# Kernel optimization log

Measured on AMD Instinct MI355X. Metric: run time of the kernel, lower is better.

## Reference

```python
import jax, jax.numpy as jnp
import numpy as np

_EPS = 1e-5
_K = 3  # spatial kernel size (partitions of adjacency)


def _build_A():
    num_node = 24
    self_link = [(i, i) for i in range(num_node)]
    neighbor = [(1, 0), (2, 0), (3, 0), (4, 1), (5, 2), (6, 3), (7, 4), (8, 5), (9, 6),
                (10, 7), (11, 8), (12, 9), (13, 9), (14, 9), (15, 12), (16, 13), (17, 14),
                (18, 16), (19, 17), (20, 18), (21, 19), (22, 20), (23, 21)]
    edges = self_link + neighbor
    Ab = np.zeros((num_node, num_node))
    for i, j in edges:
        Ab[j, i] = 1
        Ab[i, j] = 1
    max_hop = 1
    hop_dis = np.full((num_node, num_node), np.inf)
    transfer = [np.linalg.matrix_power(Ab, d) for d in range(max_hop + 1)]
    arrive = np.stack(transfer) > 0
    for d in range(max_hop, -1, -1):
        hop_dis[arrive[d]] = d
    adjacency = np.zeros((num_node, num_node))
    for hop in range(max_hop + 1):
        adjacency[hop_dis == hop] = 1
    Dl = adjacency.sum(0)
    Dn = np.zeros_like(adjacency)
    for i in range(num_node):
        if Dl[i] > 0:
            Dn[i, i] = Dl[i] ** (-1)
    AD = adjacency @ Dn
    center = 0
    As = []
    for hop in range(max_hop + 1):
        a_root = np.zeros_like(AD)
        a_close = np.zeros_like(AD)
        a_further = np.zeros_like(AD)
        for i in range(num_node):
            for j in range(num_node):
                if hop_dis[j, i] == hop:
                    if hop_dis[j, center] == hop_dis[i, center]:
                        a_root[j, i] = AD[j, i]
                    elif hop_dis[j, center] > hop_dis[i, center]:
                        a_close[j, i] = AD[j, i]
                    else:
                        a_further[j, i] = AD[j, i]
        if hop == 0:
            As.append(a_root)
        else:
            As.append(a_root + a_close)
            As.append(a_further)
    return np.stack(As).astype(np.float32)  # [3, 24, 24]


def setup_inputs() -> dict:
    key = jax.random.key(0)
    cnt = [0]
    def nk():
        cnt[0] += 1
        return jax.random.fold_in(key, cnt[0])
    def rn(shape, scale=1.0):
        return scale * jax.random.normal(nk(), shape, jnp.float32)
    B, T, N, C = 32, 256, 24, 3
    inp = {}
    inp['x'] = rn((B, T, N, C))
    inp['A'] = jnp.asarray(_build_A())
    inp['data_bn_g'] = 1.0 + 0.1 * rn((N * C,))
    inp['data_bn_b'] = 0.1 * rn((N * C,))
    for li in range(3):
        inp['ei%d' % li] = 1.0 + 0.05 * rn((_K, 24, 24))  # edge importance
    chans = [(C, 256), (256, 128), (128, 64)]
    for li, (ci, co) in enumerate(chans):
        p = 'l%d_' % li
        inp[p + 'gcn_w'] = rn((co * _K, ci), 1.0 / np.sqrt(ci))
        inp[p + 'gcn_b'] = 0.01 * rn((co * _K,))
        inp[p + 'bn1_g'] = 1.0 + 0.1 * rn((co,))
        inp[p + 'bn1_b'] = 0.1 * rn((co,))
        inp[p + 'tcn_w'] = rn((co, co, 5, 1), 1.0 / np.sqrt(co * 5))
        inp[p + 'tcn_b'] = 0.01 * rn((co,))
        inp[p + 'bn2_g'] = 1.0 + 0.1 * rn((co,))
        inp[p + 'bn2_b'] = 0.1 * rn((co,))
        if li > 0:  # residual 1x1 conv + BN when in_channels != out_channels
            inp[p + 'res_w'] = rn((co, ci), 1.0 / np.sqrt(ci))
            inp[p + 'res_b'] = 0.01 * rn((co,))
            inp[p + 'res_bn_g'] = 1.0 + 0.1 * rn((co,))
            inp[p + 'res_bn_b'] = 0.1 * rn((co,))
    inp['fcn_w'] = rn((6, 64), 1.0 / np.sqrt(64))
    inp['fcn_b'] = 0.01 * rn((6,))
    return inp


def _bn(x, g, b):
    # eval-mode BatchNorm2d, running_mean=0, running_var=1; x: [B,C,T,V]
    inv = 1.0 / np.sqrt(1.0 + _EPS)
    return x * (inv * g)[None, :, None, None] + b[None, :, None, None]


def _gcn(x, w, b, Aeff):
    # x: [B,Cin,T,V]; w: [K*Cout,Cin]; Aeff: [K,V,V]
    y = jnp.einsum('bctv,oc->botv', x, w) + b[None, :, None, None]
    Bn, KC, Tn, V = y.shape
    y = y.reshape(Bn, _K, KC // _K, Tn, V)
    return jnp.einsum('bkctv,kvw->bctw', y, Aeff)


def _tconv(x, w, b):
    # temporal conv kernel (5,1), pad (2,0); NCHW
    y = jax.lax.conv_general_dilated(x, w, window_strides=(1, 1),
                                     padding=((2, 2), (0, 0)),
                                     dimension_numbers=('NCHW', 'OIHW', 'NCHW'))
    return y + b[None, :, None, None]


def _layer(x, Aeff, gw, gb, g1, b1, tw, tb, g2, b2, res):
    y = _gcn(x, gw, gb, Aeff)
    y = jax.nn.relu(_bn(y, g1, b1))
    y = _bn(_tconv(y, tw, tb), g2, b2) + res  # dropout is identity in eval
    return jax.nn.relu(y)


def reference(x, A, data_bn_g, data_bn_b, ei0, ei1, ei2,
              l0_gcn_w, l0_gcn_b, l0_bn1_g, l0_bn1_b, l0_tcn_w, l0_tcn_b, l0_bn2_g, l0_bn2_b,
              l1_gcn_w, l1_gcn_b, l1_bn1_g, l1_bn1_b, l1_tcn_w, l1_tcn_b, l1_bn2_g, l1_bn2_b,
              l1_res_w, l1_res_b, l1_res_bn_g, l1_res_bn_b,
              l2_gcn_w, l2_gcn_b, l2_bn1_g, l2_bn1_b, l2_tcn_w, l2_tcn_b, l2_bn2_g, l2_bn2_b,
              l2_res_w, l2_res_b, l2_res_bn_g, l2_res_bn_b,
              fcn_w, fcn_b):
    B, T, N, C = x.shape
    # data_bn over N*C channels (eval mode)
    xb = x.transpose(0, 2, 3, 1).reshape(B, N * C, T)
    inv = 1.0 / np.sqrt(1.0 + _EPS)
    xb = xb * (inv * data_bn_g)[None, :, None] + data_bn_b[None, :, None]
    h = xb.reshape(B, N, C, T).transpose(0, 2, 3, 1)  # [B,C,T,V]
    # layer 0: no residual
    h = _layer(h, A * ei0, l0_gcn_w, l0_gcn_b, l0_bn1_g, l0_bn1_b,
               l0_tcn_w, l0_tcn_b, l0_bn2_g, l0_bn2_b, 0.0)
    # layer 1: 1x1 conv + BN residual (256 -> 128)
    r1 = _bn(jnp.einsum('bctv,oc->botv', h, l1_res_w) + l1_res_b[None, :, None, None],
             l1_res_bn_g, l1_res_bn_b)
    h = _layer(h, A * ei1, l1_gcn_w, l1_gcn_b, l1_bn1_g, l1_bn1_b,
               l1_tcn_w, l1_tcn_b, l1_bn2_g, l1_bn2_b, r1)
    # layer 2: 1x1 conv + BN residual (128 -> 64)
    r2 = _bn(jnp.einsum('bctv,oc->botv', h, l2_res_w) + l2_res_b[None, :, None, None],
             l2_res_bn_g, l2_res_bn_b)
    h = _layer(h, A * ei2, l2_gcn_w, l2_gcn_b, l2_bn1_g, l2_bn1_b,
               l2_tcn_w, l2_tcn_b, l2_bn2_g, l2_bn2_b, r2)
    out = jnp.einsum('bctv,oc->botv', h, fcn_w) + fcn_b[None, :, None, None]
    return out.transpose(0, 2, 3, 1)  # [B,T,V,6]
```

## Files before the change

kernel.cpp:

```cpp
#include <hip/hip_runtime.h>

typedef _Float16 half8 __attribute__((ext_vector_type(8)));
typedef _Float16 half2v __attribute__((ext_vector_type(2)));
typedef float floatx16 __attribute__((ext_vector_type(16)));

static constexpr int gT = 256;
static constexpr int gV = 24;
static constexpr int gN = gT * gV;
static constexpr float BN_INV = 0.99999500003749969f;

#define GLOAD_LDS16(g, l)                                            \
  __builtin_amdgcn_global_load_lds(                                  \
      (const __attribute__((address_space(1))) unsigned int*)(g),    \
      (__attribute__((address_space(3))) unsigned int*)(l), 16, 0, 0)

__global__ __launch_bounds__(256) void k_prep_aeff(
    const float* __restrict__ A, const float* __restrict__ e0,
    const float* __restrict__ e1, const float* __restrict__ e2,
    float* __restrict__ aeff, float* __restrict__ csum)
{
  int tid = blockIdx.x * 256 + threadIdx.x;
  if (tid < 3 * 1728) {
    int l = tid / 1728, r = tid % 1728;
    const float* e = (l == 0) ? e0 : ((l == 1) ? e1 : e2);
    aeff[tid] = A[r] * e[r];
  }
  if (tid < 3 * 72) {
    int l = tid / 72, r = tid % 72;
    int k = r / 24, w = r % 24;
    const float* e = (l == 0) ? e0 : ((l == 1) ? e1 : e2);
    float s = 0.f;
    for (int v = 0; v < 24; ++v) { int idx = (k * 24 + v) * 24 + w; s += A[idx] * e[idx]; }
    csum[tid] = s;
  }
}

__global__ __launch_bounds__(256) void k_prep_twf(
    const float* __restrict__ tw, _Float16* __restrict__ out, int CI, int KT)
{
  int g = blockIdx.x * 256 + threadIdx.x;
  int fid = g >> 6, lane = g & 63;
  int pl = fid & 1;
  int f2 = fid >> 1;
  int dt = f2 % 5;
  int f3 = f2 / 5;
  int ks = f3 & 1;
  int f4 = f3 >> 1;
  int kt = f4 % KT;
  int mt = f4 / KT;
  int m = mt * 32 + (lane & 31);
  int kb = kt * 32 + ks * 16 + ((lane >> 5) << 3);
  half8 o;
#pragma unroll
  for (int e = 0; e < 8; ++e) {
    float v = tw[((size_t)m * CI + (kb + e)) * 5 + dt];
    _Float16 h = (_Float16)v;
    o[e] = pl ? (_Float16)(v - (float)h) : h;
  }
  *(half8*)(out + ((size_t)fid * 64 + lane) * 8) = o;
}

__global__ __launch_bounds__(256) void k_pack_wz(
    const float* __restrict__ Wg, const float* __restrict__ Wr,
    _Float16* __restrict__ out, int CIN, int KT, int M3)
{
  int g = blockIdx.x * 256 + threadIdx.x;
  int fid = g >> 6, lane = g & 63;
  int pl = fid & 1;
  int ks = (fid >> 1) & 1;
  int rest = fid >> 2;
  int kt = rest % KT;
  int mt = rest / KT;
  int m = mt * 32 + (lane & 31);
  int kb = kt * 32 + ks * 16 + ((lane >> 5) << 3);
  const float* row = (m < M3) ? (Wg + (size_t)m * CIN) : (Wr + (size_t)(m - M3) * CIN);
  half8 o;
#pragma unroll
  for (int e = 0; e < 8; ++e) {
    float v = row[kb + e];
    _Float16 h = (_Float16)v;
    o[e] = pl ? (_Float16)(v - (float)h) : h;
  }
  *(half8*)(out + ((size_t)fid * 64 + lane) * 8) = o;
}

__global__ __launch_bounds__(256) void k_gcn0(
    const float* __restrict__ x,
    const float* __restrict__ aeff,
    const float* __restrict__ csum,
    const float* __restrict__ dbg, const float* __restrict__ dbb,
    const float* __restrict__ W0,
    const float* __restrict__ gb0,
    const float* __restrict__ g1, const float* __restrict__ b1,
    _Float16* __restrict__ yh, _Float16* __restrict__ yl,
    int b0)
{
  __shared__ float xbn[72];
  __shared__ float XA[216];
  __shared__ float WL[2304];
  __shared__ float tile[256 * 25];
  int t0 = blockIdx.x * 4, bl = blockIdx.y, tid = threadIdx.x;
  int b = b0 + bl;
  int c = tid;

  for (int i = tid; i < 2304; i += 256) WL[i] = W0[i];

  for (int tr = 0; tr < 4; ++tr) {
    int t = t0 + tr;
    __syncthreads();
    if (tid < 72) {
      int v = tid / 3, cin = tid % 3;
      float xv = x[(((size_t)b * gT + t) * gV + v) * 3 + cin];
      xbn[cin * 24 + v] = xv * (BN_INV * dbg[tid]) + dbb[tid];
    }
    __syncthreads();
    if (tid < 216) {
      int k = tid / 72, r = tid % 72, ci = r / 24, w = r % 24;
      const float* Ak = aeff + k * 576;
      float s = 0.f;
#pragma unroll
      for (int v = 0; v < 24; ++v) s += xbn[ci * 24 + v] * Ak[v * 24 + w];
      XA[tid] = s;
    }
    __syncthreads();

    float acc[24];
#pragma unroll
    for (int w = 0; w < 24; ++w) acc[w] = 0.f;
#pragma unroll
    for (int k = 0; k < 3; ++k) {
#pragma unroll
      for (int ci = 0; ci < 3; ++ci) {
        float wv = WL[(k * 256 + c) * 3 + ci];
#pragma unroll
        for (int w = 0; w < 24; ++w) acc[w] += wv * XA[(k * 3 + ci) * 24 + w];
      }
      float gv = gb0[k * 256 + c];
#pragma unroll
      for (int w = 0; w < 24; ++w) acc[w] += gv * csum[k * 24 + w];
    }
    float s1 = BN_INV * g1[c], o1 = b1[c];
#pragma unroll
    for (int w = 0; w < 24; ++w) tile[c * 25 + w] = fmaxf(acc[w] * s1 + o1, 0.f);
    __syncthreads();

    size_t nb = ((size_t)bl * gN + (size_t)t * 24);
    _Float16* dhB = yh + nb * 256;
    _Float16* dlB = yl + nb * 256;
#pragma unroll
    for (int it = 0; it < 3; ++it) {
      int idx = it * 256 + tid;
      int w = idx >> 5;
      int c0 = (idx & 31) * 8;
      half8 vh, vl;
#pragma unroll
      for (int q = 0; q < 8; ++q) {
        float v = tile[(c0 + q) * 25 + w];
        _Float16 hh = (_Float16)v;
        vh[q] = hh;
        vl[q] = (_Float16)(v - (float)hh);
      }
      *(half8*)(dhB + (size_t)w * 256 + c0) = vh;
      *(half8*)(dlB + (size_t)w * 256 + c0) = vl;
    }
  }
}

template <int CIN, int COUT>
__global__ __launch_bounds__(512) void k_gcnfuse(
    const _Float16* __restrict__ pH, const _Float16* __restrict__ pL,
    const _Float16* __restrict__ Wf,
    const float* __restrict__ aeffL, const float* __restrict__ csumL,
    const float* __restrict__ gb, const float* __restrict__ g1, const float* __restrict__ b1,
    _Float16* __restrict__ oH, _Float16* __restrict__ oL,
    float* __restrict__ res_out,
    int NBc)
{
  constexpr int KT = CIN / 32;
  constexpr int M = 4 * COUT;
  constexpr int M3 = 3 * COUT;
  constexpr int MT = M / 256;
  constexpr int BSTG_FL = 2 * 2 * 96 * 40 / 2;
  constexpr int ZLW = M * 25;
  constexpr int UNIW = (ZLW > BSTG_FL) ? ZLW : BSTG_FL;
  __shared__ float UNI[UNIW];
  __shared__ float AL[1728];
  __shared__ float csL[72];
  __shared__ __align__(16) _Float16 YST[24 * COUT * 2];
  _Float16* Bb = (_Float16*)UNI;
  float* ZL = UNI;

  int tid = threadIdx.x, w = tid >> 6, lane = tid & 63;
  int n0 = blockIdx.x * 96;

  for (int i = tid; i < 1728; i += 512) AL[i] = aeffL[i];
  if (tid < 72) csL[tid] = csumL[tid];

  floatx16 acc[MT][3] = {};

  uint4 pf[2];
  auto PREF = [&](int kt) {
#pragma unroll
    for (int it = 0; it < 2; ++it) {
      int task = it * 512 + tid;
      if (task < 768) {
        int row = task >> 3, pl = (task >> 2) & 1, seg = task & 3;
        pf[it] = *(const uint4*)((pl ? pL : pH) + (size_t)(n0 + row) * CIN + kt * 32 + seg * 8);
      }
    }
  };
  auto WRITE = [&](int buf) {
#pragma unroll
    for (int it = 0; it < 2; ++it) {
      int task = it * 512 + tid;
      if (task < 768) {
        int row = task >> 3, pl = (task >> 2) & 1, seg = task & 3;
        *(uint4*)(Bb + (((size_t)buf * 2 + pl) * 96 + row) * 40 + seg * 8) = pf[it];
      }
    }
  };

  PREF(0); WRITE(0); __syncthreads();
  int cur = 0;
  for (int kt = 0; kt < KT; ++kt) {
    if (kt + 1 < KT) PREF(kt + 1);
    const _Float16* BH = Bb + (size_t)(cur * 2 + 0) * 96 * 40;
    const _Float16* BL2 = Bb + (size_t)(cur * 2 + 1) * 96 * 40;
    __builtin_amdgcn_s_setprio(1);
#pragma unroll
    for (int ks = 0; ks < 2; ++ks) {
      int koff = ks * 16 + ((lane >> 5) << 3);
      int rowb = lane & 31;
      half8 bh[3], bl[3];
#pragma unroll
      for (int nf = 0; nf < 3; ++nf) {
        bh[nf] = *(const half8*)(BH + (rowb + nf * 32) * 40 + koff);
        bl[nf] = *(const half8*)(BL2 + (rowb + nf * 32) * 40 + koff);
      }
#pragma unroll
      for (int mti = 0; mti < MT; ++mti) {
        int mt = w * MT + mti;
        int fid = ((mt * KT + kt) * 2 + ks) * 2;
        half8 ah = *(const half8*)(Wf + ((size_t)fid * 64 + lane) * 8);
        half8 al = *(const half8*)(Wf + ((size_t)(fid + 1) * 64 + lane) * 8);
#pragma unroll
        for (int nf = 0; nf < 3; ++nf) {
          acc[mti][nf] = __builtin_amdgcn_mfma_f32_32x32x16_f16(ah, bh[nf], acc[mti][nf], 0, 0, 0);
          acc[mti][nf] = __builtin_amdgcn_mfma_f32_32x32x16_f16(ah, bl[nf], acc[mti][nf], 0, 0, 0);
          acc[mti][nf] = __builtin_amdgcn_mfma_f32_32x32x16_f16(al, bh[nf], acc[mti][nf], 0, 0, 0);
        }
      }
    }
    __builtin_amdgcn_s_setprio(0);
    if (kt + 1 < KT) WRITE(cur ^ 1);
    __syncthreads();
    cur ^= 1;
  }

  constexpr int SUBS = 512 / COUT;
  constexpr int WR = 24 / SUBS;
  int c = tid & (COUT - 1);
  int w0 = (tid / COUT) * WR;
  float s1 = BN_INV * g1[c], o1 = b1[c];
  float gv0 = gb[c], gv1 = gb[COUT + c], gv2 = gb[2 * COUT + c];

  for (int tr = 0; tr < 4; ++tr) {
    __syncthreads();
#pragma unroll
    for (int mti = 0; mti < MT; ++mti) {
#pragma unroll
      for (int nf = 0; nf < 3; ++nf) {
        int nloc = nf * 32 + (lane & 31) - tr * 24;
        if (nloc >= 0 && nloc < 24) {
          int mb_ = (w * MT + mti) * 32 + 4 * (lane >> 5);
#pragma unroll
          for (int r = 0; r < 16; ++r)
            ZL[(mb_ + (r & 3) + 8 * (r >> 2)) * 25 + nloc] = acc[mti][nf][r];
        }
      }
    }
    __syncthreads();
    float y[WR];
#pragma unroll
    for (int j = 0; j < WR; ++j) y[j] = 0.f;
#pragma unroll
    for (int k = 0; k < 3; ++k) {
#pragma unroll
      for (int v = 0; v < 24; ++v) {
        float zr = ZL[(k * COUT + c) * 25 + v];
        const float* ap = &AL[k * 576 + v * 24 + w0];
#pragma unroll
        for (int j = 0; j < WR; ++j) y[j] += zr * ap[j];
      }
    }
#pragma unroll
    for (int j = 0; j < WR; ++j) {
      int ww = w0 + j;
      float bias = gv0 * csL[ww] + gv1 * csL[24 + ww] + gv2 * csL[48 + ww];
      float yv = fmaxf((y[j] + bias) * s1 + o1, 0.f);
      _Float16 h = (_Float16)yv;
      YST[ww * COUT + c] = h;
      YST[24 * COUT + ww * COUT + c] = (_Float16)(yv - (float)h);
    }
    __syncthreads();
    constexpr int QT = 24 * COUT / 8;
    size_t nbase = (size_t)n0 + tr * 24;
    for (int idx = tid; idx < 2 * QT; idx += 512) {
      int plane = idx / QT, q = idx - plane * QT;
      _Float16* dst = (plane ? oL : oH) + nbase * COUT + q * 8;
      *(half8*)dst = *(half8*)(YST + plane * 24 * COUT + q * 8);
    }
    for (int idx = tid; idx < COUT * 6; idx += 512) {
      int cc = idx / 6, q = idx - cc * 6;
      float4 v4;
      v4.x = ZL[(M3 + cc) * 25 + 4 * q + 0];
      v4.y = ZL[(M3 + cc) * 25 + 4 * q + 1];
      v4.z = ZL[(M3 + cc) * 25 + 4 * q + 2];
      v4.w = ZL[(M3 + cc) * 25 + 4 * q + 3];
      *(float4*)(res_out + (size_t)cc * NBc + nbase + 4 * q) = v4;
    }
  }
}

template <int CIO, int MF, bool FUSE_FC>
__global__ __launch_bounds__(512) void k_tcn_mfma(
    const _Float16* __restrict__ yH, const _Float16* __restrict__ yL,
    const _Float16* __restrict__ Apack,
    const float* __restrict__ tb, const float* __restrict__ g2, const float* __restrict__ b2,
    const float* __restrict__ Zres,
    const float* __restrict__ rb, const float* __restrict__ rg, const float* __restrict__ rbb,
    _Float16* __restrict__ oH, _Float16* __restrict__ oL,
    const float* __restrict__ fw, const float* __restrict__ fb,
    float* __restrict__ outp, int b0,
    int NBc)
{
  constexpr int KT = CIO / 32;
  constexpr int M = CIO;
  constexpr int NWAVE_M = M / (MF * 32);
  constexpr int NWAVE_N = 8 / NWAVE_M;
  constexpr int NF = 128 / (32 * NWAVE_N);
  constexpr int NROW = 224;
  __shared__ _Float16 Bt[2][NROW * 64];
  __shared__ float scL[CIO], ofL[CIO], tbL[CIO], rscL[CIO], rofL[CIO], rbvL[CIO];
  __shared__ float fwL[FUSE_FC ? 384 : 4];
  int bx = blockIdx.x, bl = blockIdx.z;
  int tid = threadIdx.x, w = tid >> 6, lane = tid & 63;
  int wn = w % NWAVE_N, wm = w / NWAVE_N;
  int n0 = bx * 128;
  bool interior = (bx > 0) && (bx < 47);

  for (int i = tid; i < CIO; i += 512) {
    scL[i] = BN_INV * g2[i]; ofL[i] = b2[i]; tbL[i] = tb[i];
    if (Zres) { rscL[i] = BN_INV * rg[i]; rofL[i] = rbb[i]; rbvL[i] = rb[i]; }
  }
  if (FUSE_FC) { for (int i = tid; i < 384; i += 512) fwL[i] = fw[i]; }

  floatx16 acc[MF][NF] = {};
  const _Float16* ybH = yH + (size_t)bl * gN * CIO;
  const _Float16* ybL = yL + (size_t)bl * gN * CIO;
  int mt_base = wm * MF;

  auto ISSUE = [&](int kt, int buf) {
#pragma unroll
    for (int it = 0; it < 4; ++it) {
      int slot = w * 4 + it;
      if (slot < 28) {
        int T = slot * 64 + lane;
        int r = T >> 3, s = T & 7;
        int sl = s ^ (r & 7);
        int pl = sl >> 2, seg = sl & 3;
        int n = n0 - 48 + r;
        const _Float16* src = (pl ? ybL : ybH) + (size_t)n * CIO + kt * 32 + seg * 8;
        GLOAD_LDS16(src, &Bt[buf][(size_t)slot * 512]);
      }
    }
  };
  auto ISSUE_EDGE = [&](int kt, int buf) {
#pragma unroll
    for (int it = 0; it < 4; ++it) {
      int slot = w * 4 + it;
      if (slot < 28) {
        int T = slot * 64 + lane;
        int r = T >> 3, s = T & 7;
        int sl = s ^ (r & 7);
        int pl = sl >> 2, seg = sl & 3;
        int n = n0 - 48 + r;
        uint4 vv = make_uint4(0u, 0u, 0u, 0u);
        if (n >= 0 && n < gN)
          vv = *(const uint4*)((pl ? ybL : ybH) + (size_t)n * CIO + kt * 32 + seg * 8);
        *(uint4*)(&Bt[buf][(size_t)T * 8]) = vv;
      }
    }
  };
  auto COMPUTE = [&](int kt, int buf) {
    const _Float16* B = &Bt[buf][0];
    __builtin_amdgcn_s_setprio(1);
#pragma unroll
    for (int dt = 0; dt < 5; ++dt) {
#pragma unroll
      for (int ks = 0; ks < 2; ++ks) {
        int seg = ks * 2 + (lane >> 5);
        half8 bh[NF], blv[NF];
#pragma unroll
        for (int nf = 0; nf < NF; ++nf) {
          int rr = wn * (NF * 32) + nf * 32 + dt * 24 + (lane & 31);
          bh[nf]  = *(const half8*)(B + rr * 64 + (((0 + seg) ^ (rr & 7)) * 8));
          blv[nf] = *(const half8*)(B + rr * 64 + (((4 + seg) ^ (rr & 7)) * 8));
        }
#pragma unroll
        for (int mf = 0; mf < MF; ++mf) {
          int fid = ((((mt_base + mf) * KT + kt) * 2 + ks) * 5 + dt) * 2;
          half8 ah = *(const half8*)(Apack + ((size_t)fid * 64 + lane) * 8);
          half8 al = *(const half8*)(Apack + ((size_t)(fid + 1) * 64 + lane) * 8);
#pragma unroll
          for (int nf = 0; nf < NF; ++nf) {
            acc[mf][nf] = __builtin_amdgcn_mfma_f32_32x32x16_f16(ah, bh[nf], acc[mf][nf], 0, 0, 0);
            acc[mf][nf] = __builtin_amdgcn_mfma_f32_32x32x16_f16(ah, blv[nf], acc[mf][nf], 0, 0, 0);
            acc[mf][nf] = __builtin_amdgcn_mfma_f32_32x32x16_f16(al, bh[nf], acc[mf][nf], 0, 0, 0);
          }
        }
      }
    }
    __builtin_amdgcn_s_setprio(0);
  };

  if (interior) {
    ISSUE(0, 0);
    int cur = 0;
    for (int kt = 0; kt < KT; ++kt) {
      __builtin_amdgcn_sched_barrier(0);
      if (kt + 1 < KT) ISSUE(kt + 1, cur ^ 1);
      __builtin_amdgcn_sched_barrier(0);
      if (kt + 1 < KT) asm volatile("s_waitcnt vmcnt(4)" ::: "memory");
      else             asm volatile("s_waitcnt vmcnt(0)" ::: "memory");
      __builtin_amdgcn_sched_barrier(0);
      __builtin_amdgcn_s_barrier();
      __builtin_amdgcn_sched_barrier(0);
      COMPUTE(kt, cur);
      asm volatile("s_waitcnt lgkmcnt(0)" ::: "memory");
      __builtin_amdgcn_sched_barrier(0);
      __builtin_amdgcn_s_barrier();
      cur ^= 1;
    }
  } else {
    for (int kt = 0; kt < KT; ++kt) {
      __syncthreads();
      ISSUE_EDGE(kt, 0);
      __syncthreads();
      COMPUTE(kt, 0);
    }
  }

  int blgN = bl * gN;
#pragma unroll
  for (int mf = 0; mf < MF; ++mf) {
    int m32 = wm * MF * 32 + mf * 32 + 4 * (lane >> 5);
#pragma unroll
    for (int nf = 0; nf < NF; ++nf) {
      int n = n0 + wn * (NF * 32) + nf * 32 + (lane & 31);
      size_t nflat = (size_t)blgN + n;
#pragma unroll
      for (int r = 0; r < 16; ++r) {
        int co = m32 + (r & 3) + 8 * (r >> 2);
        float z = (acc[mf][nf][r] + tbL[co]) * scL[co] + ofL[co];
        if (Zres) z += (Zres[(size_t)co * NBc + nflat] + rbvL[co]) * rscL[co] + rofL[co];
        acc[mf][nf][r] = fmaxf(z, 0.f);
      }
    }
  }

  if constexpr (FUSE_FC) {
    __syncthreads();
    float* FC = (float*)&Bt[0][0];
    float p[6];
#pragma unroll
    for (int o = 0; o < 6; ++o) p[o] = 0.f;
    int m32 = wm * 32 + 4 * (lane >> 5);
#pragma unroll
    for (int r = 0; r < 16; ++r) {
      int co = m32 + (r & 3) + 8 * (r >> 2);
      float z = acc[0][0][r];
#pragma unroll
      for (int o = 0; o < 6; ++o) p[o] += fwL[o * 64 + co] * z;
    }
#pragma unroll
    for (int o = 0; o < 6; ++o) p[o] += __shfl_xor(p[o], 32);
    if (lane < 32) {
      int nloc = wn * 32 + lane;
#pragma unroll
      for (int o = 0; o < 6; ++o)
        FC[(wm * 128 + nloc) * 6 + o] = p[o];
    }
    __syncthreads();
    for (int idx = tid; idx < 768; idx += 512) {
      int nloc = idx / 6, o = idx % 6;
      float val = fb[o] + FC[nloc * 6 + o] + FC[(128 + nloc) * 6 + o];
      int n = n0 + nloc;
      int t = n / 24, v = n % 24;
      outp[(((size_t)(b0 + bl) * gT + t) * gV + v) * 6 + o] = val;
    }
  } else {
    constexpr int CPB = CIO / 2;
    constexpr int NHALF = (128 * (CPB + 1) * 4 > 2 * NROW * 64 * 2) ? 2 : 1;
    constexpr int ROWS_P = 128 / NHALF;
    constexpr int PITCH = CPB + 1;
    uint* ST = (uint*)&Bt[0][0];
    uint* oH32 = (uint*)oH;
    uint* oL32 = (uint*)oL;
    constexpr int QITERS = ROWS_P * CPB / 4 / 512;

#pragma unroll
    for (int half = 0; half < NHALF; ++half) {
#pragma unroll
      for (int pass = 0; pass < 2; ++pass) {
        __syncthreads();
        if (NHALF == 1 || wn == half) {
          int cl = wm * MF * 32;
#pragma unroll
          for (int mf = 0; mf < MF; ++mf) {
#pragma unroll
            for (int nf = 0; nf < NF; ++nf) {
              int nl = wn * (NF * 32) + nf * 32 + (lane & 31) - half * ROWS_P;
#pragma unroll
              for (int r = 0; r < 16; r += 2) {
                float z0 = acc[mf][nf][r], z1 = acc[mf][nf][r + 1];
                _Float16 a0 = (_Float16)z0, a1 = (_Float16)z1;
                if (pass == 1) { a0 = (_Float16)(z0 - (float)a0); a1 = (_Float16)(z1 - (float)a1); }
                half2v p2; p2[0] = a0; p2[1] = a1;
                int col2 = (cl + mf * 32 + 4 * (lane >> 5) + (r & 3) + 8 * (r >> 2)) >> 1;
                ST[nl * PITCH + col2] = *(uint*)&p2;
              }
            }
          }
        }
        __syncthreads();
        uint* dst = (pass == 0) ? oH32 : oL32;
#pragma unroll
        for (int i = 0; i < QITERS; ++i) {
          int idx = i * 512 + tid;
          int row = idx / (CPB / 4), c4 = (idx % (CPB / 4)) * 4;
          uint4 v;
          v.x = ST[row * PITCH + c4 + 0];
          v.y = ST[row * PITCH + c4 + 1];
          v.z = ST[row * PITCH + c4 + 2];
          v.w = ST[row * PITCH + c4 + 3];
          *(uint4*)(dst + ((size_t)blgN + n0 + half * ROWS_P + row) * (CIO / 2) + c4) = v;
        }
      }
    }
  }
}

extern "C" void kernel_launch(void* const* d_in, const int* in_sizes, int n_in,
                              void* d_out, int out_size, void* d_ws, size_t ws_size,
                              hipStream_t stream) {
  const float* x    = (const float*)d_in[0];
  const float* A    = (const float*)d_in[1];
  const float* dbg  = (const float*)d_in[2];
  const float* dbb  = (const float*)d_in[3];
  const float* ei0  = (const float*)d_in[4];
  const float* ei1  = (const float*)d_in[5];
  const float* ei2  = (const float*)d_in[6];
  const float* w0g  = (const float*)d_in[7];
  const float* gb0  = (const float*)d_in[8];
  const float* g10  = (const float*)d_in[9];
  const float* b10  = (const float*)d_in[10];
  const float* tw0  = (const float*)d_in[11];
  const float* tb0  = (const float*)d_in[12];
  const float* g20  = (const float*)d_in[13];
  const float* b20  = (const float*)d_in[14];
  const float* w1g  = (const float*)d_in[15];
  const float* gb1  = (const float*)d_in[16];
  const float* g11  = (const float*)d_in[17];
  const float* b11  = (const float*)d_in[18];
  const float* tw1  = (const float*)d_in[19];
  const float* tb1  = (const float*)d_in[20];
  const float* g21  = (const float*)d_in[21];
  const float* b21  = (const float*)d_in[22];
  const float* rw1  = (const float*)d_in[23];
  const float* rb1  = (const float*)d_in[24];
  const float* rg1  = (const float*)d_in[25];
  const float* rbb1 = (const float*)d_in[26];
  const float* w2g  = (const float*)d_in[27];
  const float* gb2  = (const float*)d_in[28];
  const float* g12  = (const float*)d_in[29];
  const float* b12  = (const float*)d_in[30];
  const float* tw2  = (const float*)d_in[31];
  const float* tb2  = (const float*)d_in[32];
  const float* g22  = (const float*)d_in[33];
  const float* b22  = (const float*)d_in[34];
  const float* rw2  = (const float*)d_in[35];
  const float* rb2  = (const float*)d_in[36];
  const float* rg2  = (const float*)d_in[37];
  const float* rbb2 = (const float*)d_in[38];
  const float* fw   = (const float*)d_in[39];
  const float* fb   = (const float*)d_in[40];
  float* outp = (float*)d_out;
  float* ws = (float*)d_ws;

  size_t off = 0;
  auto alloc = [&](size_t n) { size_t o = off; off += n; return o; };
  size_t oAE  = alloc(3 * 1728);
  size_t oCS  = alloc(3 * 72);
  size_t oA0  = alloc((size_t)1280 * 512 / 2);
  size_t oA1  = alloc((size_t)320 * 512 / 2);
  size_t oA2  = alloc((size_t)80 * 512 / 2);
  size_t oWz1 = alloc((size_t)512 * 512 / 2);
  size_t oWz2 = alloc((size_t)128 * 512 / 2);
  off = (off + 3) & ~(size_t)3;

  const size_t perBatchBytes = (size_t)gN * 640 * 4;
  int Bc = 32;
  while (Bc > 1 && off * 4 + (size_t)Bc * perBatchBytes > ws_size) Bc >>= 1;
  int NBc = Bc * gN;

  float* B1 = ws + off;
  float* B2 = B1 + (size_t)NBc * 256;
  float* Rb = B2 + (size_t)NBc * 256;
  _Float16* b1h = (_Float16*)B1;
  _Float16* b2h = (_Float16*)B2;
  _Float16* A0 = (_Float16*)(ws + oA0);
  _Float16* A1 = (_Float16*)(ws + oA1);
  _Float16* A2 = (_Float16*)(ws + oA2);
  _Float16* Wz1 = (_Float16*)(ws + oWz1);
  _Float16* Wz2 = (_Float16*)(ws + oWz2);

  k_prep_aeff<<<21, 256, 0, stream>>>(A, ei0, ei1, ei2, ws + oAE, ws + oCS);
  k_prep_twf<<<320, 256, 0, stream>>>(tw0, A0, 256, 8);
  k_prep_twf<<<80, 256, 0, stream>>>(tw1, A1, 128, 4);
  k_prep_twf<<<20, 256, 0, stream>>>(tw2, A2, 64, 2);
  k_pack_wz<<<128, 256, 0, stream>>>(w1g, rw1, Wz1, 256, 8, 384);
  k_pack_wz<<<32, 256, 0, stream>>>(w2g, rw2, Wz2, 128, 4, 192);

  for (int b0 = 0; b0 < 32; b0 += Bc) {
    k_gcn0<<<dim3(gT / 4, Bc), 256, 0, stream>>>(x, ws + oAE, ws + oCS, dbg, dbb,
                                                 w0g, gb0, g10, b10,
                                                 b1h, b1h + (size_t)NBc * 256, b0);
    k_tcn_mfma<256, 2, false><<<dim3(48, 1, Bc), 512, 0, stream>>>(
        b1h, b1h + (size_t)NBc * 256, A0, tb0, g20, b20,
        nullptr, nullptr, nullptr, nullptr,
        b2h, b2h + (size_t)NBc * 256, nullptr, nullptr, nullptr, 0, NBc);
    k_gcnfuse<256, 128><<<dim3(NBc / 96), 512, 0, stream>>>(
        b2h, b2h + (size_t)NBc * 256, Wz1,
        ws + oAE + 1728, ws + oCS + 72, gb1, g11, b11,
        b1h, b1h + (size_t)NBc * 128, Rb, NBc);
    k_tcn_mfma<128, 2, false><<<dim3(48, 1, Bc), 512, 0, stream>>>(
        b1h, b1h + (size_t)NBc * 128, A1, tb1, g21, b21,
        Rb, rb1, rg1, rbb1,
        b2h, b2h + (size_t)NBc * 128, nullptr, nullptr, nullptr, 0, NBc);
    k_gcnfuse<128, 64><<<dim3(NBc / 96), 512, 0, stream>>>(
        b2h, b2h + (size_t)NBc * 128, Wz2,
        ws + oAE + 2 * 1728, ws + oCS + 144, gb2, g12, b12,
        b1h, b1h + (size_t)NBc * 64, Rb, NBc);
    k_tcn_mfma<64, 1, true><<<dim3(48, 1, Bc), 512, 0, stream>>>(
        b1h, b1h + (size_t)NBc * 64, A2, tb2, g22, b22,
        Rb, rb2, rg2, rbb2,
        nullptr, nullptr, fw, fb, outp, b0, NBc);
  }
  (void)in_sizes; (void)n_in; (void)out_size;
}
```

Baseline: 1.323 ms.

## Double TCN tile width to 256 and drop LDS double buffering

The temporal-conv MFMA kernel now computes 256 output positions per block instead of 128. This cuts the 48-row temporal halo overhead per block and halves the grid. The double-buffered async load pipeline is replaced with a single LDS buffer and plain syncthreads between load and compute, which frees LDS for the larger tile but removes the overlap of global loads with MFMA work. The epilogue and the fused FC path are adjusted to the wider tile, and the grid shrinks to 24 blocks per batch, which may reduce occupancy and load balance.

New measurement: 1.645 ms. 24.3% more time.

```diff
diff --git a/kernel.cpp b/kernel.cpp
--- a/kernel.cpp
+++ b/kernel.cpp
@@ -336,18 +336,20 @@
 {
   constexpr int KT = CIO / 32;
   constexpr int M = CIO;
+  constexpr int N_BLK = 256;
   constexpr int NWAVE_M = M / (MF * 32);
   constexpr int NWAVE_N = 8 / NWAVE_M;
-  constexpr int NF = 128 / (32 * NWAVE_N);
-  constexpr int NROW = 224;
-  __shared__ _Float16 Bt[2][NROW * 64];
+  constexpr int NF = N_BLK / (32 * NWAVE_N);
+  constexpr int NROW = 352;
+  constexpr int NSLOT = NROW * 8;
+  __shared__ _Float16 Bt[NROW * 64];
   __shared__ float scL[CIO], ofL[CIO], tbL[CIO], rscL[CIO], rofL[CIO], rbvL[CIO];
   __shared__ float fwL[FUSE_FC ? 384 : 4];
   int bx = blockIdx.x, bl = blockIdx.z;
   int tid = threadIdx.x, w = tid >> 6, lane = tid & 63;
   int wn = w % NWAVE_N, wm = w / NWAVE_N;
-  int n0 = bx * 128;
-  bool interior = (bx > 0) && (bx < 47);
+  int n0 = bx * N_BLK;
+  bool interior = (bx > 0) && (bx < (gN / N_BLK - 1));
 
   for (int i = tid; i < CIO; i += 512) {
     scL[i] = BN_INV * g2[i]; ofL[i] = b2[i]; tbL[i] = tb[i];
@@ -360,27 +362,26 @@
   const _Float16* ybL = yL + (size_t)bl * gN * CIO;
   int mt_base = wm * MF;
 
-  auto ISSUE = [&](int kt, int buf) {
-#pragma unroll
-    for (int it = 0; it < 4; ++it) {
-      int slot = w * 4 + it;
-      if (slot < 28) {
-        int T = slot * 64 + lane;
+  auto ISSUE = [&](int kt) {
+#pragma unroll
+    for (int it = 0; it < 6; ++it) {
+      int base = it * 512 + w * 64;
+      if (base < NSLOT) {
+        int T = base + lane;
         int r = T >> 3, s = T & 7;
         int sl = s ^ (r & 7);
         int pl = sl >> 2, seg = sl & 3;
         int n = n0 - 48 + r;
         const _Float16* src = (pl ? ybL : ybH) + (size_t)n * CIO + kt * 32 + seg * 8;
-        GLOAD_LDS16(src, &Bt[buf][(size_t)slot * 512]);
+        GLOAD_LDS16(src, Bt + (size_t)base * 8);
       }
     }
   };
-  auto ISSUE_EDGE = [&](int kt, int buf) {
-#pragma unroll
-    for (int it = 0; it < 4; ++it) {
-      int slot = w * 4 + it;
-      if (slot < 28) {
-        int T = slot * 64 + lane;
+  auto ISSUE_EDGE = [&](int kt) {
+#pragma unroll
+    for (int it = 0; it < 6; ++it) {
+      int T = it * 512 + tid;
+      if (T < NSLOT) {
         int r = T >> 3, s = T & 7;
         int sl = s ^ (r & 7);
         int pl = sl >> 2, seg = sl & 3;
@@ -388,12 +389,12 @@
         uint4 vv = make_uint4(0u, 0u, 0u, 0u);
         if (n >= 0 && n < gN)
           vv = *(const uint4*)((pl ? ybL : ybH) + (size_t)n * CIO + kt * 32 + seg * 8);
-        *(uint4*)(&Bt[buf][(size_t)T * 8]) = vv;
+        *(uint4*)(Bt + (size_t)T * 8) = vv;
       }
     }
   };
-  auto COMPUTE = [&](int kt, int buf) {
-    const _Float16* B = &Bt[buf][0];
+  auto COMPUTE = [&](int kt) {
+    const _Float16* B = &Bt[0];
     __builtin_amdgcn_s_setprio(1);
 #pragma unroll
     for (int dt = 0; dt < 5; ++dt) {
@@ -424,31 +425,11 @@
     __builtin_amdgcn_s_setprio(0);
   };
 
-  if (interior) {
-    ISSUE(0, 0);
-    int cur = 0;
-    for (int kt = 0; kt < KT; ++kt) {
-      __builtin_amdgcn_sched_barrier(0);
-      if (kt + 1 < KT) ISSUE(kt + 1, cur ^ 1);
-      __builtin_amdgcn_sched_barrier(0);
-      if (kt + 1 < KT) asm volatile("s_waitcnt vmcnt(4)" ::: "memory");
-      else             asm volatile("s_waitcnt vmcnt(0)" ::: "memory");
-      __builtin_amdgcn_sched_barrier(0);
-      __builtin_amdgcn_s_barrier();
-      __builtin_amdgcn_sched_barrier(0);
-      COMPUTE(kt, cur);
-      asm volatile("s_waitcnt lgkmcnt(0)" ::: "memory");
-      __builtin_amdgcn_sched_barrier(0);
-      __builtin_amdgcn_s_barrier();
-      cur ^= 1;
-    }
-  } else {
-    for (int kt = 0; kt < KT; ++kt) {
-      __syncthreads();
-      ISSUE_EDGE(kt, 0);
-      __syncthreads();
-      COMPUTE(kt, 0);
-    }
+  for (int kt = 0; kt < KT; ++kt) {
+    __syncthreads();
+    if (interior) ISSUE(kt); else ISSUE_EDGE(kt);
+    __syncthreads();
+    COMPUTE(kt);
   }
 
   int blgN = bl * gN;
@@ -471,56 +452,60 @@
 
   if constexpr (FUSE_FC) {
     __syncthreads();
-    float* FC = (float*)&Bt[0][0];
-    float p[6];
-#pragma unroll
-    for (int o = 0; o < 6; ++o) p[o] = 0.f;
+    float* FC = (float*)&Bt[0];
     int m32 = wm * 32 + 4 * (lane >> 5);
 #pragma unroll
-    for (int r = 0; r < 16; ++r) {
-      int co = m32 + (r & 3) + 8 * (r >> 2);
-      float z = acc[0][0][r];
-#pragma unroll
-      for (int o = 0; o < 6; ++o) p[o] += fwL[o * 64 + co] * z;
-    }
-#pragma unroll
-    for (int o = 0; o < 6; ++o) p[o] += __shfl_xor(p[o], 32);
-    if (lane < 32) {
-      int nloc = wn * 32 + lane;
-#pragma unroll
-      for (int o = 0; o < 6; ++o)
-        FC[(wm * 128 + nloc) * 6 + o] = p[o];
-    }
-    __syncthreads();
-    for (int idx = tid; idx < 768; idx += 512) {
+    for (int nf = 0; nf < 2; ++nf) {
+      float p[6];
+#pragma unroll
+      for (int o = 0; o < 6; ++o) p[o] = 0.f;
+#pragma unroll
+      for (int r = 0; r < 16; ++r) {
+        int co = m32 + (r & 3) + 8 * (r >> 2);
+        float z = acc[0][nf][r];
+#pragma unroll
+        for (int o = 0; o < 6; ++o) p[o] += fwL[o * 64 + co] * z;
+      }
+#pragma unroll
+      for (int o = 0; o < 6; ++o) p[o] += __shfl_xor(p[o], 32);
+      if (lane < 32) {
+        int nloc = wn * 64 + nf * 32 + lane;
+#pragma unroll
+        for (int o = 0; o < 6; ++o)
+          FC[(wm * 256 + nloc) * 6 + o] = p[o];
+      }
+    }
+    __syncthreads();
+    for (int idx = tid; idx < 1536; idx += 512) {
       int nloc = idx / 6, o = idx % 6;
-      float val = fb[o] + FC[nloc * 6 + o] + FC[(128 + nloc) * 6 + o];
+      float val = fb[o] + FC[nloc * 6 + o] + FC[(256 + nloc) * 6 + o];
       int n = n0 + nloc;
       int t = n / 24, v = n % 24;
       outp[(((size_t)(b0 + bl) * gT + t) * gV + v) * 6 + o] = val;
     }
   } else {
     constexpr int CPB = CIO / 2;
-    constexpr int NHALF = (128 * (CPB + 1) * 4 > 2 * NROW * 64 * 2) ? 2 : 1;
-    constexpr int ROWS_P = 128 / NHALF;
+    constexpr int ROWS_P = (CIO == 256) ? 64 : 128;
+    constexpr int NSEG = N_BLK / ROWS_P;
     constexpr int PITCH = CPB + 1;
-    uint* ST = (uint*)&Bt[0][0];
+    uint* ST = (uint*)&Bt[0];
     uint* oH32 = (uint*)oH;
     uint* oL32 = (uint*)oL;
     constexpr int QITERS = ROWS_P * CPB / 4 / 512;
 
 #pragma unroll
-    for (int half = 0; half < NHALF; ++half) {
+    for (int seg = 0; seg < NSEG; ++seg) {
 #pragma unroll
       for (int pass = 0; pass < 2; ++pass) {
         __syncthreads();
-        if (NHALF == 1 || wn == half) {
-          int cl = wm * MF * 32;
-#pragma unroll
-          for (int mf = 0; mf < MF; ++mf) {
-#pragma unroll
-            for (int nf = 0; nf < NF; ++nf) {
-              int nl = wn * (NF * 32) + nf * 32 + (lane & 31) - half * ROWS_P;
+        int cl = wm * MF * 32;
+#pragma unroll
+        for (int mf = 0; mf < MF; ++mf) {
+#pragma unroll
+          for (int nf = 0; nf < NF; ++nf) {
+            int rbase = wn * (NF * 32) + nf * 32;
+            if (rbase >= seg * ROWS_P && rbase < (seg + 1) * ROWS_P) {
+              int nl = rbase + (lane & 31) - seg * ROWS_P;
 #pragma unroll
               for (int r = 0; r < 16; r += 2) {
                 float z0 = acc[mf][nf][r], z1 = acc[mf][nf][r + 1];
@@ -544,7 +529,7 @@
           v.y = ST[row * PITCH + c4 + 1];
           v.z = ST[row * PITCH + c4 + 2];
           v.w = ST[row * PITCH + c4 + 3];
-          *(uint4*)(dst + ((size_t)blgN + n0 + half * ROWS_P + row) * (CIO / 2) + c4) = v;
+          *(uint4*)(dst + ((size_t)blgN + n0 + seg * ROWS_P + row) * (CIO / 2) + c4) = v;
         }
       }
     }
@@ -636,7 +621,7 @@
     k_gcn0<<<dim3(gT / 4, Bc), 256, 0, stream>>>(x, ws + oAE, ws + oCS, dbg, dbb,
                                                  w0g, gb0, g10, b10,
                                                  b1h, b1h + (size_t)NBc * 256, b0);
-    k_tcn_mfma<256, 2, false><<<dim3(48, 1, Bc), 512, 0, stream>>>(
+    k_tcn_mfma<256, 2, false><<<dim3(24, 1, Bc), 512, 0, stream>>>(
         b1h, b1h + (size_t)NBc * 256, A0, tb0, g20, b20,
         nullptr, nullptr, nullptr, nullptr,
         b2h, b2h + (size_t)NBc * 256, nullptr, nullptr, nullptr, 0, NBc);
@@ -644,7 +629,7 @@
         b2h, b2h + (size_t)NBc * 256, Wz1,
         ws + oAE + 1728, ws + oCS + 72, gb1, g11, b11,
         b1h, b1h + (size_t)NBc * 128, Rb, NBc);
-    k_tcn_mfma<128, 2, false><<<dim3(48, 1, Bc), 512, 0, stream>>>(
+    k_tcn_mfma<128, 2, false><<<dim3(24, 1, Bc), 512, 0, stream>>>(
         b1h, b1h + (size_t)NBc * 128, A1, tb1, g21, b21,
         Rb, rb1, rg1, rbb1,
         b2h, b2h + (size_t)NBc * 128, nullptr, nullptr, nullptr, 0, NBc);
@@ -652,7 +637,7 @@
         b2h, b2h + (size_t)NBc * 128, Wz2,
         ws + oAE + 2 * 1728, ws + oCS + 144, gb2, g12, b12,
         b1h, b1h + (size_t)NBc * 64, Rb, NBc);
-    k_tcn_mfma<64, 1, true><<<dim3(48, 1, Bc), 512, 0, stream>>>(
+    k_tcn_mfma<64, 1, true><<<dim3(24, 1, Bc), 512, 0, stream>>>(
         b1h, b1h + (size_t)NBc * 64, A2, tb2, g22, b22,
         Rb, rb2, rg2, rbb2,
         nullptr, nullptr, fw, fb, outp, b0, NBc);
```

## Stage GCN operand tiles with direct global-to-LDS loads and XOR-swizzled layout

Applied to the files above, without the earlier changes.

Replaces the register-staged prefetch (global load into registers, then LDS store) in the fused GCN GEMM with global_load_lds DMA straight into a double-buffered LDS tile. It uses an XOR-swizzled, unpadded slot layout to avoid bank conflicts, and manual vmcnt waits plus barriers to overlap the next tile's load with the current MFMA work. This removes register pressure and LDS write instructions. The cost is fragile hand-written waitcnt logic that depends on per-wave load counts.

Result: faster. 1.249 ms (-5.6%).

```diff
diff --git a/kernel.cpp b/kernel.cpp
--- a/kernel.cpp
+++ b/kernel.cpp
@@ -180,7 +180,8 @@
   constexpr int M = 4 * COUT;
   constexpr int M3 = 3 * COUT;
   constexpr int MT = M / 256;
-  constexpr int BSTG_FL = 2 * 2 * 96 * 40 / 2;
+  constexpr int NSLOT = 96 * 8;
+  constexpr int BSTG_FL = 2 * NSLOT * 4;
   constexpr int ZLW = M * 25;
   constexpr int UNIW = (ZLW > BSTG_FL) ? ZLW : BSTG_FL;
   __shared__ float UNI[UNIW];
@@ -198,44 +199,32 @@
 
   floatx16 acc[MT][3] = {};
 
-  uint4 pf[2];
-  auto PREF = [&](int kt) {
+  auto ISSUE = [&](int kt, int buf) {
 #pragma unroll
     for (int it = 0; it < 2; ++it) {
-      int task = it * 512 + tid;
-      if (task < 768) {
-        int row = task >> 3, pl = (task >> 2) & 1, seg = task & 3;
-        pf[it] = *(const uint4*)((pl ? pL : pH) + (size_t)(n0 + row) * CIN + kt * 32 + seg * 8);
+      int base = it * 512 + w * 64;
+      if (base < NSLOT) {
+        int T = base + lane;
+        int r = T >> 3, s = T & 7;
+        int sl = s ^ (r & 7);
+        int pl = sl >> 2, seg = sl & 3;
+        const _Float16* src = (pl ? pL : pH) + (size_t)(n0 + r) * CIN + kt * 32 + seg * 8;
+        GLOAD_LDS16(src, Bb + ((size_t)buf * NSLOT + base) * 8);
       }
     }
   };
-  auto WRITE = [&](int buf) {
-#pragma unroll
-    for (int it = 0; it < 2; ++it) {
-      int task = it * 512 + tid;
-      if (task < 768) {
-        int row = task >> 3, pl = (task >> 2) & 1, seg = task & 3;
-        *(uint4*)(Bb + (((size_t)buf * 2 + pl) * 96 + row) * 40 + seg * 8) = pf[it];
-      }
-    }
-  };
-
-  PREF(0); WRITE(0); __syncthreads();
-  int cur = 0;
-  for (int kt = 0; kt < KT; ++kt) {
-    if (kt + 1 < KT) PREF(kt + 1);
-    const _Float16* BH = Bb + (size_t)(cur * 2 + 0) * 96 * 40;
-    const _Float16* BL2 = Bb + (size_t)(cur * 2 + 1) * 96 * 40;
+  auto COMPUTE = [&](int kt, int buf) {
+    const _Float16* B = Bb + (size_t)buf * NSLOT * 8;
     __builtin_amdgcn_s_setprio(1);
 #pragma unroll
     for (int ks = 0; ks < 2; ++ks) {
-      int koff = ks * 16 + ((lane >> 5) << 3);
-      int rowb = lane & 31;
+      int seg = ks * 2 + (lane >> 5);
       half8 bh[3], bl[3];
 #pragma unroll
       for (int nf = 0; nf < 3; ++nf) {
-        bh[nf] = *(const half8*)(BH + (rowb + nf * 32) * 40 + koff);
-        bl[nf] = *(const half8*)(BL2 + (rowb + nf * 32) * 40 + koff);
+        int rr = (lane & 31) + nf * 32;
+        bh[nf] = *(const half8*)(B + rr * 64 + (((0 + seg) ^ (rr & 7)) * 8));
+        bl[nf] = *(const half8*)(B + rr * 64 + (((4 + seg) ^ (rr & 7)) * 8));
       }
 #pragma unroll
       for (int mti = 0; mti < MT; ++mti) {
@@ -252,8 +241,27 @@
       }
     }
     __builtin_amdgcn_s_setprio(0);
-    if (kt + 1 < KT) WRITE(cur ^ 1);
-    __syncthreads();
+  };
+
+  ISSUE(0, 0);
+  int cur = 0;
+  for (int kt = 0; kt < KT; ++kt) {
+    __builtin_amdgcn_sched_barrier(0);
+    if (kt + 1 < KT) ISSUE(kt + 1, cur ^ 1);
+    __builtin_amdgcn_sched_barrier(0);
+    if (kt + 1 < KT) {
+      if (w < 4) asm volatile("s_waitcnt vmcnt(2)" ::: "memory");
+      else       asm volatile("s_waitcnt vmcnt(1)" ::: "memory");
+    } else {
+      asm volatile("s_waitcnt vmcnt(0)" ::: "memory");
+    }
+    __builtin_amdgcn_sched_barrier(0);
+    __builtin_amdgcn_s_barrier();
+    __builtin_amdgcn_sched_barrier(0);
+    COMPUTE(kt, cur);
+    asm volatile("s_waitcnt lgkmcnt(0)" ::: "memory");
+    __builtin_amdgcn_sched_barrier(0);
+    __builtin_amdgcn_s_barrier();
     cur ^= 1;
   }
 
```
